# Optimization experiments

Hardware: AMD Instinct MI355X
Metric: run time of the kernel (lower is better)

Reference implementation:

```python
import jax, jax.numpy as jnp
import numpy as np

BETA = 0.25  # commitment_beta


def setup_inputs() -> dict:
    key = jax.random.key(0)
    k1, k2 = jax.random.split(key)
    x = jax.random.normal(k1, (16, 256, 32, 32), dtype=jnp.float32)
    # codebook weight: (n_embed + 1, embed_dim); last row is the padding idx (zeros)
    weight = jax.random.normal(k2, (8193, 256), dtype=jnp.float32) * 0.05
    weight = weight.at[-1].set(0.0)
    return {"x": x, "weight": weight}


def reference(x, weight):
    # Eval-mode forward of VectorQuantize2 (accept_image_fmap=True, no EMA update).
    B, C, H, W = x.shape
    xf = jnp.transpose(x, (0, 2, 3, 1)).reshape(B, H * W, C)  # b (h w) c
    emb = weight[:-1]  # [N, C], drop padding row
    # squared euclidean distance; argmin identical to torch.cdist argmin
    d2 = (
        jnp.sum(xf * xf, axis=-1, keepdims=True)
        - 2.0 * jnp.einsum("bnc,kc->bnk", xf, emb)
        + jnp.sum(emb * emb, axis=-1)
    )  # [B, HW, N]
    code = jnp.argmin(d2, axis=-1)  # [B, HW]
    x_q = emb[code]  # [B, HW, C]
    loss = BETA * jnp.mean((jax.lax.stop_gradient(x_q) - xf) ** 2) + jnp.mean(
        (x_q - jax.lax.stop_gradient(xf)) ** 2
    )
    # straight-through estimator
    xq_st = xf + jax.lax.stop_gradient(x_q - xf)
    xq_out = jnp.transpose(xq_st.reshape(B, H, W, C), (0, 3, 1, 2))  # b c h w
    code_out = code.reshape(B, H, W)
    return xq_out, loss, code_out
```

## Files before the change

kernel.cpp:

```cpp
#include <hip/hip_runtime.h>
#include <hip/hip_bf16.h>


#define N_ROWS   16384
#define KCODES   8192
#define DIM      256
#define LOSS_OFF 4194304
#define CODE_OFF 4194305
#define MARGIN_ACC 0.005f

typedef _Float16 half8  __attribute__((ext_vector_type(8)));
typedef _Float16 half4v __attribute__((ext_vector_type(4)));
typedef float    float4v __attribute__((ext_vector_type(4)));
typedef unsigned long long u64;

__device__ __forceinline__ unsigned umax32(unsigned a, unsigned b) { return a > b ? a : b; }
__device__ __forceinline__ unsigned umin32(unsigned a, unsigned b) { return a < b ? a : b; }
__device__ __forceinline__ u64 umax64(u64 a, u64 b) { return a > b ? a : b; }
__device__ __forceinline__ u64 umin64(u64 a, u64 b) { return a < b ? a : b; }
__device__ __forceinline__ void gll16(const _Float16* g, _Float16* l) {
  __builtin_amdgcn_global_load_lds((const __attribute__((address_space(1))) void*)g,
                                   (__attribute__((address_space(3))) void*)l, 16, 0, 0);
}


__global__ __launch_bounds__(256) void k_prep_x(const float* __restrict__ x, _Float16* __restrict__ xh) {
  int t   = threadIdx.x;
  int blk = blockIdx.x;
  int row = t & 63;
  int s   = t >> 6;
  int r   = blk * 64 + row;
  int b   = r >> 10;
  int n   = r & 1023;
  const float* xb = x + (size_t)b * 262144 + n;
  int r7 = r & 7, rl = r & 127;
  size_t tb = (size_t)(r >> 7) * 32768;
  for (int j = 0; j < 8; ++j) {
    int g = s + 4 * j;
    int chunk = g >> 3, kg = g & 7;
    half8 h;
#pragma unroll
    for (int i = 0; i < 8; ++i) h[i] = (_Float16)xb[(size_t)(g * 8 + i) * 1024];
    int p = kg ^ r7;
    *(half8*)&xh[tb + (size_t)chunk * 8192 + rl * 64 + p * 8] = h;
  }
}

__global__ __launch_bounds__(256) void k_prep_e(const float* __restrict__ wt, _Float16* __restrict__ eh,
                                                float* __restrict__ en2c) {
  __shared__ __align__(16) _Float16 ls[8192];
  __shared__ float es[32];
  int t = threadIdx.x;
  int k0 = blockIdx.x * 32;
  if (t < 32) es[t] = 0.f;
  __syncthreads();
  const float* wb = wt + (size_t)k0 * 256;
  for (int i = 0; i < 8; ++i) {
    int lin = i * 1024 + t * 4;
    float4v v = *(const float4v*)&wb[lin];
    half4v h; float ss = 0.f;
#pragma unroll
    for (int j = 0; j < 4; ++j) { h[j] = (_Float16)v[j]; ss = fmaf(v[j], v[j], ss); }
    *(half4v*)&ls[lin] = h;
    atomicAdd(&es[lin >> 8], ss);
  }
  __syncthreads();
  size_t tb = (size_t)(k0 >> 7) * 32768;
  for (int i = 0; i < 4; ++i) {
    int u = i * 256 + t;
    int code_l = u >> 5;
    int cu = u & 31, chunk = cu >> 3, p = cu & 7;
    int kgl = k0 + code_l;
    int kg = p ^ (kgl & 7);
    half8 h = *(half8*)&ls[code_l * 256 + chunk * 64 + kg * 8];
    *(half8*)&eh[tb + (size_t)chunk * 8192 + (size_t)(kgl & 127) * 64 + p * 8] = h;
  }
  if (t < 32) en2c[k0 + t] = 32.0f - 0.5f * es[t];
}

__global__ __launch_bounds__(256) void k_gemm(const _Float16* __restrict__ xh, const _Float16* __restrict__ eh,
                                              const float* __restrict__ en2c,
                                              u64* __restrict__ top2) {
  __shared__ __align__(16) _Float16 As[8192];
  __shared__ __align__(16) _Float16 Bs[8192];
  int t    = threadIdx.x;
  int bx   = blockIdx.x;
  int by   = blockIdx.y;
  int lane = t & 63, w = t >> 6;
  int wr = w & 1, wc = w >> 1;
  int ln15 = lane & 15, q = lane >> 4;
  int q4 = q * 4;

  const _Float16* Ag = eh + (size_t)bx * 32768;
  const _Float16* Bg = xh + (size_t)by * 32768;

  int kwave = bx * 128 + wr * 64;
  float4v cin[4];
#pragma unroll
  for (int mi = 0; mi < 4; ++mi) cin[mi] = *(const float4v*)&en2c[kwave + mi * 16 + q4];

  float4v acc[4][4];
#pragma unroll
  for (int mi = 0; mi < 4; ++mi)
#pragma unroll
    for (int ni = 0; ni < 4; ++ni) acc[mi][ni] = cin[mi];

  int so = (w * 64 + lane) * 8;
  int lo = w * 512;

  for (int ch = 0; ch < 4; ++ch) {
    if (ch) __syncthreads();
    const _Float16* ac = Ag + ch * 8192;
    const _Float16* bc = Bg + ch * 8192;
#pragma unroll
    for (int i = 0; i < 4; ++i) {
      gll16(ac + i * 2048 + so, As + i * 2048 + lo);
      gll16(bc + i * 2048 + so, Bs + i * 2048 + lo);
    }
    __syncthreads();
#pragma unroll
    for (int ks = 0; ks < 2; ++ks) {
      half8 af[4], bf[4];
#pragma unroll
      for (int mi = 0; mi < 4; ++mi) {
        int row = wr * 64 + mi * 16 + ln15;
        af[mi] = *(const half8*)&As[(row * 8 + ((ks * 4 + q) ^ (row & 7))) * 8];
      }
#pragma unroll
      for (int ni = 0; ni < 4; ++ni) {
        int row = wc * 64 + ni * 16 + ln15;
        bf[ni] = *(const half8*)&Bs[(row * 8 + ((ks * 4 + q) ^ (row & 7))) * 8];
      }
#pragma unroll
      for (int mi = 0; mi < 4; ++mi)
#pragma unroll
        for (int ni = 0; ni < 4; ++ni)
          acc[mi][ni] = __builtin_amdgcn_mfma_f32_16x16x32_f16(af[mi], bf[ni], acc[mi][ni], 0, 0, 0);
    }
  }

  __syncthreads();
  u64* ep = (u64*)(void*)As;

#pragma unroll
  for (int ni = 0; ni < 4; ++ni) {
    unsigned hi[8], lo2[8];
#pragma unroll
    for (int j = 0; j < 8; ++j) {
      int mi = j >> 1, rb = (j & 1) * 2;
      unsigned p0 = (__float_as_uint(acc[mi][ni][rb])     & 0xFFFFFFC0u) | (unsigned)(mi * 16 + q4 + rb);
      unsigned p1 = (__float_as_uint(acc[mi][ni][rb + 1]) & 0xFFFFFFC0u) | (unsigned)(mi * 16 + q4 + rb + 1);
      hi[j] = umax32(p0, p1); lo2[j] = umin32(p0, p1);
    }
#pragma unroll
    for (int st = 4; st; st >>= 1)
#pragma unroll
      for (int j = 0; j < 8; ++j) if (j < st) {
        unsigned nb = umax32(hi[j], hi[j + st]);
        unsigned ns = umax32(umin32(hi[j], hi[j + st]), umax32(lo2[j], lo2[j + st]));
        hi[j] = nb; lo2[j] = ns;
      }
    unsigned b = hi[0], s = lo2[0];
#pragma unroll
    for (int d = 16; d < 64; d <<= 1) {
      unsigned ob = __shfl_xor(b, d);
      unsigned os = __shfl_xor(s, d);
      unsigned ns = umax32(umin32(b, ob), umax32(s, os));
      b = umax32(b, ob); s = ns;
    }
    if (q == 0) {
      int rl = wc * 64 + ni * 16 + ln15;
      ep[rl * 4 + wr * 2 + 0] = ((u64)b << 32) | (unsigned)(kwave + (b & 63));
      ep[rl * 4 + wr * 2 + 1] = ((u64)s << 32) | (unsigned)(kwave + (s & 63));
    }
  }
  __syncthreads();
  if (t < 128) {
    u64 a0 = ep[t * 4 + 0], a1 = ep[t * 4 + 1], b0 = ep[t * 4 + 2], b1 = ep[t * 4 + 3];
    u64 nb = umax64(a0, b0);
    u64 ns = umax64(umin64(a0, b0), umax64(a1, b1));
    size_t rowg = (size_t)by * 128 + t;
    top2[rowg * 128 + bx * 2 + 0] = nb;
    top2[rowg * 128 + bx * 2 + 1] = ns;
  }
}

__global__ __launch_bounds__(256) void k_refine(const u64* __restrict__ top2,
                                                const float* __restrict__ x, const float* __restrict__ w,
                                                int* __restrict__ code, float* __restrict__ out) {
  int t = threadIdx.x, lane = t & 63, wv = t >> 6;
  int row = blockIdx.x * 4 + wv;
  const u64* tr = top2 + (size_t)row * 128;
  u64 e0 = tr[2 * lane], e1 = tr[2 * lane + 1];
  u64 mx = umax64(e0, e1);
#pragma unroll
  for (int d = 1; d < 64; d <<= 1) mx = umax64(mx, __shfl_xor(mx, d));
  float fm = __uint_as_float((unsigned)(mx >> 32) & 0xFFFFFFC0u);
  bool c0 = __uint_as_float((unsigned)(e0 >> 32) & 0xFFFFFFC0u) >= fm - MARGIN_ACC;
  bool c1 = __uint_as_float((unsigned)(e1 >> 32) & 0xFFFFFFC0u) >= fm - MARGIN_ACC;
  u64 bal0 = __ballot(c0), bal1 = __ballot(c1);
  int kbest;
  if (__popcll(bal0) + __popcll(bal1) <= 1) {
    kbest = (int)(unsigned)(mx & 0xffffffffULL);
  } else {
    int b = row >> 10, n = row & 1023;
    const float* xr = x + (size_t)b * 262144 + n;
    float4v ex;
#pragma unroll
    for (int i = 0; i < 4; ++i) ex[i] = xr[(size_t)(lane * 4 + i) * 1024];
    double bs = 1e300; int bk = 0x7fffffff;
    for (int pass = 0; pass < 2; ++pass) {
      u64 bal = pass ? bal1 : bal0;
      u64 src = pass ? e1 : e0;
      while (bal) {
        int l = __ffsll((unsigned long long)bal) - 1;
        bal &= bal - 1;
        int kc = (int)(unsigned)(__shfl(src, l) & 0xffffffffULL);
        float4v wv4 = *(const float4v*)&w[(size_t)kc * DIM + lane * 4];
        double s = 0.0;
#pragma unroll
        for (int i = 0; i < 4; ++i) { double e = (double)wv4[i]; s += e * (e - 2.0 * (double)ex[i]); }
#pragma unroll
        for (int d = 1; d < 64; d <<= 1) s += __shfl_xor(s, d);
        if (s < bs || (s == bs && kc < bk)) { bs = s; bk = kc; }
      }
    }
    kbest = bk;
  }
  if (lane == 0) { code[row] = kbest; out[CODE_OFF + row] = (float)kbest; }
}

__global__ __launch_bounds__(256) void k_out(const int* __restrict__ code, const float* __restrict__ w,
                                             const float* __restrict__ x, float* __restrict__ out,
                                             float* __restrict__ lacc) {
  __shared__ float ec[32 * 261];
  __shared__ int   cds[32];
  __shared__ float part[4];
  int t   = threadIdx.x;
  int blk = blockIdx.x;
  int row0 = blk * 32;
  int b = row0 >> 10, n0 = row0 & 1023;
  if (t < 32) cds[t] = code[row0 + t];
  __syncthreads();
  {
    int rr = t >> 6;
    int c4 = (t & 63) * 4;
    for (int j = 0; j < 8; ++j) {
      int r = rr + 4 * j;
      float4v v = *(const float4v*)&w[(size_t)cds[r] * DIM + c4];
#pragma unroll
      for (int i = 0; i < 4; ++i) ec[r * 261 + c4 + i] = v[i];
    }
  }
  __syncthreads();
  float ls = 0.f;
  int r2 = t & 31;
  int cg = t >> 5;
  const size_t base = (size_t)b * 262144 + n0 + r2;
  for (int j = 0; j < 32; ++j) {
    int c = cg * 32 + j;
    float v  = ec[r2 * 261 + c];
    size_t a = base + (size_t)c * 1024;
    float xv = x[a];
    out[a] = v;
    float d = v - xv;
    ls = fmaf(d, d, ls);
  }
#pragma unroll
  for (int d = 32; d; d >>= 1) ls += __shfl_xor(ls, d);
  if ((t & 63) == 0) part[t >> 6] = ls;
  __syncthreads();
  if (t == 0) atomicAdd(lacc, part[0] + part[1] + part[2] + part[3]);
}

__global__ void k_loss(const float* __restrict__ lacc, float* __restrict__ out) {
  out[LOSS_OFF] = 1.25f * (*lacc) / 4194304.0f;
}

extern "C" void kernel_launch(void* const* d_in, const int* in_sizes, int n_in,
                              void* d_out, int out_size, void* d_ws, size_t ws_size,
                              hipStream_t stream) {
  const float* x = (const float*)d_in[0];
  const float* w = (const float*)d_in[1];
  float* out = (float*)d_out;
  char* ws = (char*)d_ws;
  _Float16* xh  = (_Float16*)(ws);
  _Float16* eh  = (_Float16*)(ws + 8388608);
  float*    en2c = (float*)(ws + 12582912);
  int*      codep = (int*)(ws + 12615680);
  float*    lacc  = (float*)(ws + 12681216);
  u64*      top2  = (u64*)d_out;

  hipMemsetAsync(lacc, 0, 4, stream);
  k_prep_x<<<256, 256, 0, stream>>>(x, xh);
  k_prep_e<<<256, 256, 0, stream>>>(w, eh, en2c);
  k_gemm<<<dim3(64, 128), 256, 0, stream>>>(xh, eh, en2c, top2);
  k_refine<<<4096, 256, 0, stream>>>(top2, x, w, codep, out);
  k_out<<<512, 256, 0, stream>>>(codep, w, x, out, lacc);
  k_loss<<<1, 1, 0, stream>>>(lacc, out);
}
```

Before: 185.7 us.

## Fuse prep kernels, pack top-2 into 32-bit keys, merge refine with output

Combines the x and codebook prep kernels into one launch and replaces the LDS atomic row-norm sum with wave shuffles. The GEMM epilogue now packs both best and second-best candidates per 128-code tile into a single 64-bit word with a 7-bit local index, which halves the top-2 buffer and moves it from the output buffer to workspace. Refinement, gather/output and the loss reduction are merged into one kernel, and a last-block atomic counter finalizes the loss. This cuts three launches and some intermediate traffic, at the cost of coarser score quantization (one more mantissa bit dropped) and a slightly wider margin that may send more rows to the fp64 refine path.

```diff
diff --git a/kernel.cpp b/kernel.cpp
--- a/kernel.cpp
+++ b/kernel.cpp
@@ -7,7 +7,7 @@
 #define DIM      256
 #define LOSS_OFF 4194304
 #define CODE_OFF 4194305
-#define MARGIN_ACC 0.005f
+#define MARGIN_ACC 0.006f
 
 typedef _Float16 half8  __attribute__((ext_vector_type(8)));
 typedef _Float16 half4v __attribute__((ext_vector_type(4)));
@@ -16,66 +16,66 @@
 
 __device__ __forceinline__ unsigned umax32(unsigned a, unsigned b) { return a > b ? a : b; }
 __device__ __forceinline__ unsigned umin32(unsigned a, unsigned b) { return a < b ? a : b; }
-__device__ __forceinline__ u64 umax64(u64 a, u64 b) { return a > b ? a : b; }
-__device__ __forceinline__ u64 umin64(u64 a, u64 b) { return a < b ? a : b; }
 __device__ __forceinline__ void gll16(const _Float16* g, _Float16* l) {
   __builtin_amdgcn_global_load_lds((const __attribute__((address_space(1))) void*)g,
                                    (__attribute__((address_space(3))) void*)l, 16, 0, 0);
 }
 
 
-__global__ __launch_bounds__(256) void k_prep_x(const float* __restrict__ x, _Float16* __restrict__ xh) {
-  int t   = threadIdx.x;
-  int blk = blockIdx.x;
-  int row = t & 63;
-  int s   = t >> 6;
-  int r   = blk * 64 + row;
-  int b   = r >> 10;
-  int n   = r & 1023;
-  const float* xb = x + (size_t)b * 262144 + n;
-  int r7 = r & 7, rl = r & 127;
-  size_t tb = (size_t)(r >> 7) * 32768;
-  for (int j = 0; j < 8; ++j) {
-    int g = s + 4 * j;
-    int chunk = g >> 3, kg = g & 7;
-    half8 h;
-#pragma unroll
-    for (int i = 0; i < 8; ++i) h[i] = (_Float16)xb[(size_t)(g * 8 + i) * 1024];
-    int p = kg ^ r7;
-    *(half8*)&xh[tb + (size_t)chunk * 8192 + rl * 64 + p * 8] = h;
-  }
-}
-
-__global__ __launch_bounds__(256) void k_prep_e(const float* __restrict__ wt, _Float16* __restrict__ eh,
-                                                float* __restrict__ en2c) {
+__global__ __launch_bounds__(256) void k_prep(const float* __restrict__ x, _Float16* __restrict__ xh,
+                                              const float* __restrict__ wt, _Float16* __restrict__ eh,
+                                              float* __restrict__ en2c) {
   __shared__ __align__(16) _Float16 ls[8192];
   __shared__ float es[32];
   int t = threadIdx.x;
-  int k0 = blockIdx.x * 32;
-  if (t < 32) es[t] = 0.f;
-  __syncthreads();
-  const float* wb = wt + (size_t)k0 * 256;
-  for (int i = 0; i < 8; ++i) {
-    int lin = i * 1024 + t * 4;
-    float4v v = *(const float4v*)&wb[lin];
-    half4v h; float ss = 0.f;
-#pragma unroll
-    for (int j = 0; j < 4; ++j) { h[j] = (_Float16)v[j]; ss = fmaf(v[j], v[j], ss); }
-    *(half4v*)&ls[lin] = h;
-    atomicAdd(&es[lin >> 8], ss);
-  }
-  __syncthreads();
-  size_t tb = (size_t)(k0 >> 7) * 32768;
-  for (int i = 0; i < 4; ++i) {
-    int u = i * 256 + t;
-    int code_l = u >> 5;
-    int cu = u & 31, chunk = cu >> 3, p = cu & 7;
-    int kgl = k0 + code_l;
-    int kg = p ^ (kgl & 7);
-    half8 h = *(half8*)&ls[code_l * 256 + chunk * 64 + kg * 8];
-    *(half8*)&eh[tb + (size_t)chunk * 8192 + (size_t)(kgl & 127) * 64 + p * 8] = h;
-  }
-  if (t < 32) en2c[k0 + t] = 32.0f - 0.5f * es[t];
+  if (blockIdx.x < 256) {
+    int blk = blockIdx.x;
+    int row = t & 63;
+    int s   = t >> 6;
+    int r   = blk * 64 + row;
+    int b   = r >> 10;
+    int n   = r & 1023;
+    const float* xb = x + (size_t)b * 262144 + n;
+    int r7 = r & 7, rl = r & 127;
+    size_t tb = (size_t)(r >> 7) * 32768;
+    for (int j = 0; j < 8; ++j) {
+      int g = s + 4 * j;
+      int chunk = g >> 3, kg = g & 7;
+      half8 h;
+#pragma unroll
+      for (int i = 0; i < 8; ++i) h[i] = (_Float16)xb[(size_t)(g * 8 + i) * 1024];
+      int p = kg ^ r7;
+      *(half8*)&xh[tb + (size_t)chunk * 8192 + rl * 64 + p * 8] = h;
+    }
+  } else {
+    int blk  = blockIdx.x - 256;
+    int lane = t & 63, wv = t >> 6;
+    int k0 = blk * 32;
+    const float* wb = wt + (size_t)k0 * 256;
+    for (int i = 0; i < 8; ++i) {
+      int lin = i * 1024 + t * 4;
+      float4v v = *(const float4v*)&wb[lin];
+      half4v h; float ss = 0.f;
+#pragma unroll
+      for (int j = 0; j < 4; ++j) { h[j] = (_Float16)v[j]; ss = fmaf(v[j], v[j], ss); }
+      *(half4v*)&ls[lin] = h;
+#pragma unroll
+      for (int d = 32; d; d >>= 1) ss += __shfl_xor(ss, d);
+      if (lane == 0) es[i * 4 + wv] = ss;
+    }
+    __syncthreads();
+    size_t tb = (size_t)(k0 >> 7) * 32768;
+    for (int i = 0; i < 4; ++i) {
+      int u = i * 256 + t;
+      int code_l = u >> 5;
+      int cu = u & 31, chunk = cu >> 3, p = cu & 7;
+      int kgl = k0 + code_l;
+      int kg = p ^ (kgl & 7);
+      half8 h = *(half8*)&ls[code_l * 256 + chunk * 64 + kg * 8];
+      *(half8*)&eh[tb + (size_t)chunk * 8192 + (size_t)(kgl & 127) * 64 + p * 8] = h;
+    }
+    if (t < 32) en2c[k0 + t] = 32.0f - 0.5f * es[t];
+  }
 }
 
 __global__ __launch_bounds__(256) void k_gemm(const _Float16* __restrict__ xh, const _Float16* __restrict__ eh,
@@ -141,6 +141,7 @@
 
   __syncthreads();
   u64* ep = (u64*)(void*)As;
+  int ibase = wr * 64 + q4;
 
 #pragma unroll
   for (int ni = 0; ni < 4; ++ni) {
@@ -148,8 +149,8 @@
 #pragma unroll
     for (int j = 0; j < 8; ++j) {
       int mi = j >> 1, rb = (j & 1) * 2;
-      unsigned p0 = (__float_as_uint(acc[mi][ni][rb])     & 0xFFFFFFC0u) | (unsigned)(mi * 16 + q4 + rb);
-      unsigned p1 = (__float_as_uint(acc[mi][ni][rb + 1]) & 0xFFFFFFC0u) | (unsigned)(mi * 16 + q4 + rb + 1);
+      unsigned p0 = (__float_as_uint(acc[mi][ni][rb])     & 0xFFFFFF80u) | (unsigned)(ibase + mi * 16 + rb);
+      unsigned p1 = (__float_as_uint(acc[mi][ni][rb + 1]) & 0xFFFFFF80u) | (unsigned)(ibase + mi * 16 + rb + 1);
       hi[j] = umax32(p0, p1); lo2[j] = umin32(p0, p1);
     }
 #pragma unroll
@@ -170,78 +171,79 @@
     }
     if (q == 0) {
       int rl = wc * 64 + ni * 16 + ln15;
-      ep[rl * 4 + wr * 2 + 0] = ((u64)b << 32) | (unsigned)(kwave + (b & 63));
-      ep[rl * 4 + wr * 2 + 1] = ((u64)s << 32) | (unsigned)(kwave + (s & 63));
+      ep[rl * 2 + wr] = ((u64)b << 32) | s;
     }
   }
   __syncthreads();
   if (t < 128) {
-    u64 a0 = ep[t * 4 + 0], a1 = ep[t * 4 + 1], b0 = ep[t * 4 + 2], b1 = ep[t * 4 + 3];
-    u64 nb = umax64(a0, b0);
-    u64 ns = umax64(umin64(a0, b0), umax64(a1, b1));
-    size_t rowg = (size_t)by * 128 + t;
-    top2[rowg * 128 + bx * 2 + 0] = nb;
-    top2[rowg * 128 + bx * 2 + 1] = ns;
-  }
-}
-
-__global__ __launch_bounds__(256) void k_refine(const u64* __restrict__ top2,
-                                                const float* __restrict__ x, const float* __restrict__ w,
-                                                int* __restrict__ code, float* __restrict__ out) {
-  int t = threadIdx.x, lane = t & 63, wv = t >> 6;
-  int row = blockIdx.x * 4 + wv;
-  const u64* tr = top2 + (size_t)row * 128;
-  u64 e0 = tr[2 * lane], e1 = tr[2 * lane + 1];
-  u64 mx = umax64(e0, e1);
-#pragma unroll
-  for (int d = 1; d < 64; d <<= 1) mx = umax64(mx, __shfl_xor(mx, d));
-  float fm = __uint_as_float((unsigned)(mx >> 32) & 0xFFFFFFC0u);
-  bool c0 = __uint_as_float((unsigned)(e0 >> 32) & 0xFFFFFFC0u) >= fm - MARGIN_ACC;
-  bool c1 = __uint_as_float((unsigned)(e1 >> 32) & 0xFFFFFFC0u) >= fm - MARGIN_ACC;
-  u64 bal0 = __ballot(c0), bal1 = __ballot(c1);
-  int kbest;
-  if (__popcll(bal0) + __popcll(bal1) <= 1) {
-    kbest = (int)(unsigned)(mx & 0xffffffffULL);
-  } else {
-    int b = row >> 10, n = row & 1023;
-    const float* xr = x + (size_t)b * 262144 + n;
-    float4v ex;
-#pragma unroll
-    for (int i = 0; i < 4; ++i) ex[i] = xr[(size_t)(lane * 4 + i) * 1024];
-    double bs = 1e300; int bk = 0x7fffffff;
-    for (int pass = 0; pass < 2; ++pass) {
-      u64 bal = pass ? bal1 : bal0;
-      u64 src = pass ? e1 : e0;
-      while (bal) {
-        int l = __ffsll((unsigned long long)bal) - 1;
-        bal &= bal - 1;
-        int kc = (int)(unsigned)(__shfl(src, l) & 0xffffffffULL);
-        float4v wv4 = *(const float4v*)&w[(size_t)kc * DIM + lane * 4];
-        double s = 0.0;
-#pragma unroll
-        for (int i = 0; i < 4; ++i) { double e = (double)wv4[i]; s += e * (e - 2.0 * (double)ex[i]); }
-#pragma unroll
-        for (int d = 1; d < 64; d <<= 1) s += __shfl_xor(s, d);
-        if (s < bs || (s == bs && kc < bk)) { bs = s; bk = kc; }
-      }
-    }
-    kbest = bk;
-  }
-  if (lane == 0) { code[row] = kbest; out[CODE_OFF + row] = (float)kbest; }
-}
-
-__global__ __launch_bounds__(256) void k_out(const int* __restrict__ code, const float* __restrict__ w,
-                                             const float* __restrict__ x, float* __restrict__ out,
-                                             float* __restrict__ lacc) {
+    u64 A = ep[t * 2 + 0], B = ep[t * 2 + 1];
+    unsigned a0 = (unsigned)(A >> 32), a1 = (unsigned)A;
+    unsigned b0 = (unsigned)(B >> 32), b1 = (unsigned)B;
+    unsigned best = umax32(a0, b0);
+    unsigned sec  = umax32(umin32(a0, b0), umax32(a1, b1));
+    top2[((size_t)by * 128 + t) * 64 + bx] = ((u64)best << 32) | sec;
+  }
+}
+
+__global__ __launch_bounds__(256) void k_refine_out(const u64* __restrict__ top2,
+                                                    const float* __restrict__ x, const float* __restrict__ w,
+                                                    float* __restrict__ out,
+                                                    float* __restrict__ lacc, unsigned* __restrict__ cnt) {
   __shared__ float ec[32 * 261];
   __shared__ int   cds[32];
   __shared__ float part[4];
-  int t   = threadIdx.x;
-  int blk = blockIdx.x;
+  int t    = threadIdx.x;
+  int lane = t & 63, wv = t >> 6;
+  int blk  = blockIdx.x;
   int row0 = blk * 32;
   int b = row0 >> 10, n0 = row0 & 1023;
-  if (t < 32) cds[t] = code[row0 + t];
-  __syncthreads();
+
+  for (int j = 0; j < 8; ++j) {
+    int rl  = wv + 4 * j;
+    int row = row0 + rl;
+    u64 e = top2[(size_t)row * 64 + lane];
+    unsigned hi = (unsigned)(e >> 32), lo = (unsigned)e;
+    unsigned mx = hi;
+#pragma unroll
+    for (int d = 1; d < 64; d <<= 1) mx = umax32(mx, __shfl_xor(mx, d));
+    float fm = __uint_as_float(mx & 0xFFFFFF80u);
+    float th = fm - MARGIN_ACC;
+    bool c0 = __uint_as_float(hi & 0xFFFFFF80u) >= th;
+    bool c1 = __uint_as_float(lo & 0xFFFFFF80u) >= th;
+    u64 bal0 = __ballot(c0), bal1 = __ballot(c1);
+    int kbest;
+    if (__popcll(bal0) + __popcll(bal1) <= 1) {
+      int l0 = __ffsll((unsigned long long)__ballot(hi == mx)) - 1;
+      kbest = l0 * 128 + (int)(__shfl(hi, l0) & 127u);
+    } else {
+      int n = row & 1023;
+      const float* xr = x + (size_t)b * 262144 + n;
+      float4v ex;
+#pragma unroll
+      for (int i = 0; i < 4; ++i) ex[i] = xr[(size_t)(lane * 4 + i) * 1024];
+      double bs = 1e300; int bk = 0x7fffffff;
+      for (int pass = 0; pass < 2; ++pass) {
+        u64 bal = pass ? bal1 : bal0;
+        unsigned src = pass ? lo : hi;
+        while (bal) {
+          int l = __ffsll((unsigned long long)bal) - 1;
+          bal &= bal - 1;
+          int kc = l * 128 + (int)(__shfl(src, l) & 127u);
+          float4v wv4 = *(const float4v*)&w[(size_t)kc * DIM + lane * 4];
+          double s = 0.0;
+#pragma unroll
+          for (int i = 0; i < 4; ++i) { double ev = (double)wv4[i]; s += ev * (ev - 2.0 * (double)ex[i]); }
+#pragma unroll
+          for (int d = 1; d < 64; d <<= 1) s += __shfl_xor(s, d);
+          if (s < bs || (s == bs && kc < bk)) { bs = s; bk = kc; }
+        }
+      }
+      kbest = bk;
+    }
+    if (lane == 0) { cds[rl] = kbest; out[CODE_OFF + row] = (float)kbest; }
+  }
+  __syncthreads();
+
   {
     int rr = t >> 6;
     int c4 = (t & 63) * 4;
@@ -268,13 +270,17 @@
   }
 #pragma unroll
   for (int d = 32; d; d >>= 1) ls += __shfl_xor(ls, d);
-  if ((t & 63) == 0) part[t >> 6] = ls;
-  __syncthreads();
-  if (t == 0) atomicAdd(lacc, part[0] + part[1] + part[2] + part[3]);
-}
-
-__global__ void k_loss(const float* __restrict__ lacc, float* __restrict__ out) {
-  out[LOSS_OFF] = 1.25f * (*lacc) / 4194304.0f;
+  if (lane == 0) part[wv] = ls;
+  __syncthreads();
+  if (t == 0) {
+    atomicAdd(lacc, part[0] + part[1] + part[2] + part[3]);
+    __threadfence();
+    unsigned old = atomicAdd(cnt, 1u);
+    if (old == 511u) {
+      __threadfence();
+      out[LOSS_OFF] = 1.25f * (*(volatile float*)lacc) / 4194304.0f;
+    }
+  }
 }
 
 extern "C" void kernel_launch(void* const* d_in, const int* in_sizes, int n_in,
@@ -284,18 +290,15 @@
   const float* w = (const float*)d_in[1];
   float* out = (float*)d_out;
   char* ws = (char*)d_ws;
-  _Float16* xh  = (_Float16*)(ws);
-  _Float16* eh  = (_Float16*)(ws + 8388608);
+  _Float16* xh   = (_Float16*)(ws);
+  _Float16* eh   = (_Float16*)(ws + 8388608);
   float*    en2c = (float*)(ws + 12582912);
-  int*      codep = (int*)(ws + 12615680);
-  float*    lacc  = (float*)(ws + 12681216);
-  u64*      top2  = (u64*)d_out;
-
-  hipMemsetAsync(lacc, 0, 4, stream);
-  k_prep_x<<<256, 256, 0, stream>>>(x, xh);
-  k_prep_e<<<256, 256, 0, stream>>>(w, eh, en2c);
+  u64*      top2 = (u64*)(ws + 12615680);
+  float*    lacc = (float*)(ws + 21004288);
+  unsigned* cnt  = (unsigned*)(ws + 21004292);
+
+  hipMemsetAsync(lacc, 0, 8, stream);
+  k_prep<<<512, 256, 0, stream>>>(x, xh, w, eh, en2c);
   k_gemm<<<dim3(64, 128), 256, 0, stream>>>(xh, eh, en2c, top2);
-  k_refine<<<4096, 256, 0, stream>>>(top2, x, w, codep, out);
-  k_out<<<512, 256, 0, stream>>>(codep, w, x, out, lacc);
-  k_loss<<<1, 1, 0, stream>>>(lacc, out);
-}
+  k_refine_out<<<512, 256, 0, stream>>>(top2, x, w, out, lacc, cnt);
+}
```

After: 190.1 us. 1.02x slower.
